# Optimization experiments

Measured on AMD Instinct MI355X. Metric: run time of the kernel, lower is better.

## Reference

```python
import jax, jax.numpy as jnp
import numpy as np

GRID_H, GRID_W = 128, 128
MODES1, MODES2 = 24, 24
DEPTH = 4
WIDTH = 64
IN_CH = 3
OUT_CH = 1
B, N = 8, 16384
EPS = 1e-5


def _gelu(x):
    return jax.nn.gelu(x, approximate=False)  # torch default (erf) GELU


def setup_inputs() -> dict:
    key = jax.random.key(0)
    ks = jax.random.split(key, 16)
    f32 = jnp.float32

    def lin(k, i, o, std=None):
        s = std if std is not None else 1.0 / np.sqrt(i)
        return (jax.random.normal(k, (i, o), f32) * s).astype(f32)

    scale = 1.0 / (WIDTH * WIDTH)
    sw_shape = (DEPTH, WIDTH, WIDTH, MODES1, MODES2)
    return {
        'coords': jax.random.uniform(ks[0], (B, N, 2), f32, -1.0, 1.0),
        'features': jax.random.normal(ks[1], (B, N, IN_CH), f32),
        'dw0': lin(ks[2], 2, 32), 'db0': jnp.zeros((32,), f32),
        'dw1': lin(ks[3], 32, 32), 'db1': jnp.zeros((32,), f32),
        'dw2': lin(ks[4], 32, 2, std=0.01), 'db2': jnp.zeros((2,), f32),
        'lift_w': lin(ks[5], IN_CH + 2, WIDTH), 'lift_b': jnp.zeros((WIDTH,), f32),
        'sw1r': scale * jax.random.uniform(ks[6], sw_shape, f32),
        'sw1i': scale * jax.random.uniform(ks[7], sw_shape, f32),
        'sw2r': scale * jax.random.uniform(ks[8], sw_shape, f32),
        'sw2i': scale * jax.random.uniform(ks[9], sw_shape, f32),
        'pw_w': (jax.random.normal(ks[10], (DEPTH, WIDTH, WIDTH), f32) / np.sqrt(WIDTH)).astype(f32),
        'pw_b': jnp.zeros((DEPTH, WIDTH), f32),
        'p1_w': lin(ks[11], WIDTH, 128), 'p1_b': jnp.zeros((128,), f32),
        'p2_w': lin(ks[12], 128, OUT_CH), 'p2_b': jnp.zeros((OUT_CH,), f32),
    }


def _spectral_conv2d(x, w1, w2):
    # x: (B, C, H, W); w1/w2: (C_in, C_out, MODES1, MODES2) complex
    Bb, C, H, W = x.shape
    x_ft = jnp.fft.rfft2(x)  # (B, C, H, W//2+1)
    lo = jnp.einsum('bixy,ioxy->boxy', x_ft[:, :, :MODES1, :MODES2], w1)
    hi = jnp.einsum('bixy,ioxy->boxy', x_ft[:, :, -MODES1:, :MODES2], w2)
    out_ft = jnp.zeros((Bb, WIDTH, H, W // 2 + 1), jnp.complex64)
    out_ft = out_ft.at[:, :, :MODES1, :MODES2].set(lo)
    out_ft = out_ft.at[:, :, -MODES1:, :MODES2].set(hi)
    return jnp.fft.irfft2(out_ft, s=(H, W))


def _forward(coords, features, dw0, db0, dw1, db1, dw2, db2, lift_w, lift_b,
             sw1r, sw1i, sw2r, sw2i, pw_w, pw_b, p1_w, p1_b, p2_w, p2_b):
    Bb, Nn, _ = coords.shape
    # 1) deformation: latent = x + MLP(x), clamped to [-1, 1]
    h = _gelu(coords @ dw0 + db0)
    h = _gelu(h @ dw1 + db1)
    latent = jnp.clip(coords + (h @ dw2 + db2), -1.0, 1.0)
    # 2) lifting on concat(features, coords)
    feat = jnp.concatenate([features, coords], axis=-1) @ lift_w + lift_b  # (B,N,width)
    # 3) P2G: nearest-neighbor scatter-mean onto latent grid (align_corners=True)
    ph = (latent[..., 0] + 1.0) * 0.5 * (GRID_H - 1)
    pw = (latent[..., 1] + 1.0) * 0.5 * (GRID_W - 1)
    ih = jnp.clip(jnp.round(ph).astype(jnp.int32), 0, GRID_H - 1)
    iw = jnp.clip(jnp.round(pw).astype(jnp.int32), 0, GRID_W - 1)
    boff = jnp.arange(Bb, dtype=jnp.int32)[:, None] * (GRID_H * GRID_W)
    flat = (boff + ih * GRID_W + iw).reshape(-1)
    nseg = Bb * GRID_H * GRID_W
    sums = jax.ops.segment_sum(feat.reshape(-1, WIDTH), flat, num_segments=nseg)
    cnts = jax.ops.segment_sum(jnp.ones((Bb * Nn, 1), feat.dtype), flat, num_segments=nseg)
    grid = (sums / jnp.maximum(cnts, 1.0)).reshape(Bb, GRID_H, GRID_W, WIDTH)
    grid = grid.transpose(0, 3, 1, 2)  # (B, width, H, W)
    # 4) FNO blocks: gelu(instnorm(spectral(x) + pointwise(x)))
    for d in range(DEPTH):
        w1 = sw1r[d] + 1j * sw1i[d]
        w2 = sw2r[d] + 1j * sw2i[d]
        y = _spectral_conv2d(grid, w1, w2)
        y = y + jnp.einsum('bihw,io->bohw', grid, pw_w[d]) + pw_b[d][None, :, None, None]
        mu = y.mean(axis=(2, 3), keepdims=True)
        var = y.var(axis=(2, 3), keepdims=True)
        grid = _gelu((y - mu) * jax.lax.rsqrt(var + EPS))
    # 5) G2P: bilinear sample latent grid at latent coords
    h0 = jnp.floor(ph)
    w0 = jnp.floor(pw)
    th = (ph - h0)[:, None, :]
    tw = (pw - w0)[:, None, :]
    h0i = jnp.clip(h0.astype(jnp.int32), 0, GRID_H - 1)
    h1i = jnp.clip(h0i + 1, 0, GRID_H - 1)
    w0i = jnp.clip(w0.astype(jnp.int32), 0, GRID_W - 1)
    w1i = jnp.clip(w0i + 1, 0, GRID_W - 1)
    gridf = grid.reshape(Bb, WIDTH, GRID_H * GRID_W)

    def gather(hi_, wi_):
        idx = (hi_ * GRID_W + wi_)[:, None, :]  # (B,1,N)
        return jnp.take_along_axis(gridf, idx, axis=2)  # (B,width,N)

    v00 = gather(h0i, w0i)
    v01 = gather(h0i, w1i)
    v10 = gather(h1i, w0i)
    v11 = gather(h1i, w1i)
    sampled = (v00 * (1 - th) * (1 - tw) + v01 * (1 - th) * tw
               + v10 * th * (1 - tw) + v11 * th * tw)
    sampled = sampled.transpose(0, 2, 1)  # (B,N,width)
    # 6) projection (dropout is identity at eval)
    out = _gelu(sampled @ p1_w + p1_b) @ p2_w + p2_b
    return out  # (B, N, out_channels)


def reference(coords, features, dw0, db0, dw1, db1, dw2, db2, lift_w, lift_b,
              sw1r, sw1i, sw2r, sw2i, pw_w, pw_b, p1_w, p1_b, p2_w, p2_b):
    return _forward(coords, features, dw0, db0, dw1, db1, dw2, db2, lift_w, lift_b,
                    sw1r, sw1i, sw2r, sw2i, pw_w, pw_b, p1_w, p1_b, p2_w, p2_b)
```

## Files before the change

kernel.cpp:

```cpp
#include <hip/hip_runtime.h>
#include <math.h>

#define GH 128
#define GW 128
#define HWC 16384
#define NMODE 1152
#define PI_F 3.14159265358979323846f

typedef _Float16 f16;
typedef __attribute__((ext_vector_type(8))) _Float16 f16x8;
typedef __attribute__((ext_vector_type(4))) float f32x4;

__device__ __forceinline__ float gelu_f(float x) {
  return 0.5f * x * (1.0f + erff(x * 0.70710678118654752f));
}

__global__ __launch_bounds__(256) void k_twiddle(f16* __restrict__ Fw, f16* __restrict__ Fh,
                                                 f16* __restrict__ Bh, f16* __restrict__ Bw,
                                                 const float* __restrict__ p1w, f16* __restrict__ p1t)
{
  int idx = blockIdx.x * 256 + threadIdx.x;
  if (idx < 6144) {
    int n = idx >> 7, w = idx & 127;
    int ky = n >> 1;
    int ang = (ky * w) & 127;
    float s, c; sincosf((float)ang * (PI_F / 64.f), &s, &c);
    Fw[idx] = (f16)((n & 1) ? -s : c);
  } else if (idx < 18432) {
    int t = idx - 6144;
    int n = t >> 7, h = t & 127;
    int kx = n < 48 ? n : n - 48;
    int f = kx < 24 ? kx : kx + 80;
    int ang = (f * h) & 127;
    float s, c; sincosf((float)ang * (PI_F / 64.f), &s, &c);
    float v = (n < 48) ? c : s;
    Fh[t] = (f16)v;
    Bh[h * 96 + n] = (f16)v;
  } else if (idx < 26624) {
    int t = idx - 18432;
    int w = t >> 6, k = t & 63;
    float v = 0.f;
    if (k < 48 && k != 1) {
      int ky = k >> 1;
      float g = (ky == 0) ? 1.f : 2.f;
      int ang = (ky * w) & 127;
      float s, c; sincosf((float)ang * (PI_F / 64.f), &s, &c);
      v = (k & 1) ? -g * s : g * c;
    }
    Bw[t] = (f16)v;
  } else if (idx < 34816) {
    int t = idx - 26624;
    int j = t >> 6, i = t & 63;
    p1t[t] = (f16)p1w[i * 128 + j];
  }
}

__global__ __launch_bounds__(256) void k_points(
    const float* __restrict__ coords,
    const float* __restrict__ dw0, const float* __restrict__ db0,
    const float* __restrict__ dw1, const float* __restrict__ db1,
    const float* __restrict__ dw2, const float* __restrict__ db2,
    int* __restrict__ cnt_i,
    int* __restrict__ ptrank, int* __restrict__ pd_cell,
    int* __restrict__ pd_idx, float* __restrict__ pd_th, float* __restrict__ pd_tw)
{
  int pid = blockIdx.x * 256 + threadIdx.x;
  float2 c = ((const float2*)coords)[pid];

  float h1[32];
#pragma unroll
  for (int j = 0; j < 32; ++j)
    h1[j] = gelu_f(fmaf(c.x, dw0[j], fmaf(c.y, dw0[32 + j], db0[j])));

  float a[32];
#pragma unroll
  for (int j = 0; j < 32; ++j) a[j] = db1[j];
#pragma unroll 4
  for (int k = 0; k < 32; ++k) {
    float hk = h1[k];
    const float* wr = dw1 + k * 32;
#pragma unroll
    for (int j = 0; j < 32; ++j) a[j] = fmaf(hk, wr[j], a[j]);
  }

  float d0 = db2[0], d1 = db2[1];
#pragma unroll 4
  for (int k = 0; k < 32; ++k) {
    float hk = gelu_f(a[k]);
    d0 = fmaf(hk, dw2[2 * k], d0);
    d1 = fmaf(hk, dw2[2 * k + 1], d1);
  }

  float l0 = fminf(fmaxf(c.x + d0, -1.f), 1.f);
  float l1 = fminf(fmaxf(c.y + d1, -1.f), 1.f);
  float ph = (l0 + 1.f) * 0.5f * 127.f;
  float pw = (l1 + 1.f) * 0.5f * 127.f;
  int ih = min(max((int)rintf(ph), 0), 127);
  int iw = min(max((int)rintf(pw), 0), 127);
  int b = pid >> 14;
  int cell = b * HWC + ih * GW + iw;

  int r = atomicAdd(&cnt_i[cell], 1);
  ptrank[pid] = r;
  pd_cell[pid] = cell;

  float fh = floorf(ph), fw = floorf(pw);
  int h0i = min(max((int)fh, 0), 127), w0i = min(max((int)fw, 0), 127);
  pd_idx[pid] = h0i | (w0i << 8);
  pd_th[pid] = ph - fh;
  pd_tw[pid] = pw - fw;
}

__global__ __launch_bounds__(256) void k_scanA(const int* __restrict__ cnt,
                                               int* __restrict__ starts, int* __restrict__ btot)
{
  __shared__ int sh[256];
  int blk = blockIdx.x, t = threadIdx.x;
  int base = blk * 512;
  int v0 = cnt[base + 2 * t], v1 = cnt[base + 2 * t + 1];
  int pair = v0 + v1;
  sh[t] = pair; __syncthreads();
  int acc = pair;
  for (int off = 1; off < 256; off <<= 1) {
    int add = (t >= off) ? sh[t - off] : 0;
    __syncthreads();
    acc += add; sh[t] = acc;
    __syncthreads();
  }
  int excl = acc - pair;
  starts[base + 2 * t] = excl;
  starts[base + 2 * t + 1] = excl + v0;
  if (t == 255) btot[blk] = acc;
}

__global__ __launch_bounds__(256) void k_scanB(const int* __restrict__ btot, int* __restrict__ boff)
{
  __shared__ int sh[256];
  int t = threadIdx.x;
  int v = btot[t];
  sh[t] = v; __syncthreads();
  int acc = v;
  for (int off = 1; off < 256; off <<= 1) {
    int add = (t >= off) ? sh[t - off] : 0;
    __syncthreads();
    acc += add; sh[t] = acc;
    __syncthreads();
  }
  boff[t] = acc - v;
}

__global__ __launch_bounds__(256) void k_perm(const int* __restrict__ pd_cell, const int* __restrict__ ptrank,
                                              const int* __restrict__ starts, const int* __restrict__ boff,
                                              const int* __restrict__ pd_idx, const float* __restrict__ pd_th,
                                              const float* __restrict__ pd_tw,
                                              const float* __restrict__ coords, const float* __restrict__ feats,
                                              int4* __restrict__ pds,
                                              float4* __restrict__ scA, float* __restrict__ scB)
{
  int pid = blockIdx.x * 256 + threadIdx.x;
  int cell = pd_cell[pid];
  int dst = starts[cell] + boff[cell >> 9] + ptrank[pid];
  int4 rec;
  rec.x = pid;
  rec.y = pd_idx[pid];
  rec.z = __float_as_int(pd_th[pid]);
  rec.w = __float_as_int(pd_tw[pid]);
  pds[dst] = rec;
  float2 c = ((const float2*)coords)[pid];
  scA[dst] = make_float4(feats[pid * 3], feats[pid * 3 + 1], feats[pid * 3 + 2], c.x);
  scB[dst] = c.y;
}

__global__ __launch_bounds__(256) void k_gridlift(const float4* __restrict__ scA, const float* __restrict__ scB,
                                                  const int* __restrict__ starts, const int* __restrict__ boff,
                                                  const int* __restrict__ cnt_i,
                                                  const float* __restrict__ lw,
                                                  const float* __restrict__ lb,
                                                  f16* __restrict__ Gh)
{
  __shared__ float sp[2][128][5];
  __shared__ float s_lw[5][64];
  __shared__ float s_lb[64];
  __shared__ float s_cnt[128];
  int b = blockIdx.y, cbase = blockIdx.x * 128, tid = threadIdx.x;
  int cl = tid & 127, par = tid >> 7;
  int gcell = b * HWC + cbase + cl;
  int start = starts[gcell] + boff[gcell >> 9];
  int cnt = cnt_i[gcell];
  float a0 = 0.f, a1 = 0.f, a2 = 0.f, a3 = 0.f, a4 = 0.f;
  for (int p = start + par; p < start + cnt; p += 2) {
    float4 A = scA[p];
    a0 += A.x; a1 += A.y; a2 += A.z; a3 += A.w; a4 += scB[p];
  }
  sp[par][cl][0] = a0; sp[par][cl][1] = a1; sp[par][cl][2] = a2;
  sp[par][cl][3] = a3; sp[par][cl][4] = a4;
  if (par == 0) s_cnt[cl] = (float)cnt;
  for (int l = tid; l < 320; l += 256) ((float*)s_lw)[l] = lw[l];
  if (tid < 64) s_lb[tid] = lb[tid];
  __syncthreads();
  float v0 = sp[0][cl][0] + sp[1][cl][0];
  float v1 = sp[0][cl][1] + sp[1][cl][1];
  float v2 = sp[0][cl][2] + sp[1][cl][2];
  float v3 = sp[0][cl][3] + sp[1][cl][3];
  float v4 = sp[0][cl][4] + sp[1][cl][4];
  float cntf = s_cnt[cl];
  float inv = 1.f / fmaxf(cntf, 1.f);
  int oh = tid >> 7;
#pragma unroll
  for (int j = 0; j < 32; ++j) {
    int o = oh * 32 + j;
    float val = cntf * s_lb[o];
    val = fmaf(v0, s_lw[0][o], val);
    val = fmaf(v1, s_lw[1][o], val);
    val = fmaf(v2, s_lw[2][o], val);
    val = fmaf(v3, s_lw[3][o], val);
    val = fmaf(v4, s_lw[4][o], val);
    Gh[(size_t)(b * 64 + o) * HWC + cbase + cl] = (f16)(val * inv);
  }
}

__global__ __launch_bounds__(256) void k_fwdpw(const f16* __restrict__ Gh,
                                               const f16* __restrict__ Fw_t, const f16* __restrict__ Fh_t,
                                               float2* __restrict__ Xf2,
                                               const float* __restrict__ pww, const float* __restrict__ pwb,
                                               f16* __restrict__ yh)
{
  __shared__ char smem[52224];
  int tid = threadIdx.x;
  int wave = tid >> 6, lane = tid & 63, lr = lane & 15, lg = lane >> 4;

  if (blockIdx.x < 512) {
    f16 (*s_fw)[136]  = (f16(*)[136])smem;
    f16 (*s_img)[136] = (f16(*)[136])(smem + 13056);
    f16 (*s_xw)[136]  = (f16(*)[136])(smem + 13056);
    f16 (*s_fh)[136]  = (f16(*)[136])(smem + 13056 + 48 * 136 * 2);
    int bc = blockIdx.x;
    for (int l = tid; l < 2048; l += 256) {
      int r = l >> 4, c = l & 15;
      *(f16x8*)&s_img[r][c * 8] = *(const f16x8*)(Gh + (size_t)bc * HWC + r * 128 + c * 8);
    }
    for (int l = tid; l < 768; l += 256) {
      int r = l >> 4, c = l & 15;
      *(f16x8*)&s_fw[r][c * 8] = *(const f16x8*)(Fw_t + r * 128 + c * 8);
    }
    __syncthreads();

    f32x4 acc1[2][3] = {};
#pragma unroll
    for (int ks = 0; ks < 4; ++ks) {
      f16x8 a[2], b[3];
#pragma unroll
      for (int mm = 0; mm < 2; ++mm) a[mm] = *(const f16x8*)&s_img[(wave * 2 + mm) * 16 + lr][ks * 32 + lg * 8];
#pragma unroll
      for (int nt = 0; nt < 3; ++nt) b[nt] = *(const f16x8*)&s_fw[nt * 16 + lr][ks * 32 + lg * 8];
#pragma unroll
      for (int mm = 0; mm < 2; ++mm)
#pragma unroll
        for (int nt = 0; nt < 3; ++nt)
          acc1[mm][nt] = __builtin_amdgcn_mfma_f32_16x16x32_f16(a[mm], b[nt], acc1[mm][nt], 0, 0, 0);
    }
    __syncthreads();
#pragma unroll
    for (int mm = 0; mm < 2; ++mm)
#pragma unroll
      for (int nt = 0; nt < 3; ++nt) {
        int n = nt * 16 + lr;
        int h0 = (wave * 2 + mm) * 16 + lg * 4;
#pragma unroll
        for (int r = 0; r < 4; ++r) s_xw[n][h0 + r] = (f16)acc1[mm][nt][r];
      }
    for (int l = tid; l < 1536; l += 256) {
      int r = l >> 4, c = l & 15;
      *(f16x8*)&s_fh[r][c * 8] = *(const f16x8*)(Fh_t + r * 128 + c * 8);
    }
    __syncthreads();

    for (int u = wave; u < 9; u += 4) {
      int mt = u / 3, ntC = u - mt * 3;
      f32x4 accC = {}, accS = {};
#pragma unroll
      for (int ks = 0; ks < 4; ++ks) {
        f16x8 a  = *(const f16x8*)&s_xw[mt * 16 + lr][ks * 32 + lg * 8];
        f16x8 bC = *(const f16x8*)&s_fh[ntC * 16 + lr][ks * 32 + lg * 8];
        f16x8 bS = *(const f16x8*)&s_fh[(ntC + 3) * 16 + lr][ks * 32 + lg * 8];
        accC = __builtin_amdgcn_mfma_f32_16x16x32_f16(a, bC, accC, 0, 0, 0);
        accS = __builtin_amdgcn_mfma_f32_16x16x32_f16(a, bS, accS, 0, 0, 0);
      }
      int kx = ntC * 16 + lr;
      int ky0 = (mt * 16 + lg * 4) >> 1;
      Xf2[bc * NMODE + kx * 24 + ky0]     = make_float2(accC[0] + accS[1], accC[1] - accS[0]);
      Xf2[bc * NMODE + kx * 24 + ky0 + 1] = make_float2(accC[2] + accS[3], accC[3] - accS[2]);
    }
  } else {
    f16 (*gt)[72] = (f16(*)[72])smem;
    f16 (*wt)[72] = (f16(*)[72])(smem + 36864);
    float* s_b    = (float*)(smem + 46080);
    int blk = blockIdx.x - 512;
    int b = blk >> 6, p0 = (blk & 63) * 256;
    for (int l = tid; l < 4096; l += 256) {
      int i = l >> 6, o = l & 63;
      wt[o][i ^ (((o >> 3) & 7) << 3)] = (f16)pww[l];
    }
    if (tid < 64) s_b[tid] = pwb[tid];
    for (int l = tid; l < 2048; l += 256) {
      int i = l >> 5, pc = (l & 31) * 8;
      f16x8 v = *(const f16x8*)(Gh + (size_t)(b * 64 + i) * HWC + p0 + pc);
      int sw = (l & 7) << 3;
#pragma unroll
      for (int j = 0; j < 8; ++j) gt[pc + j][i ^ sw] = v[j];
    }
    __syncthreads();
    int pw_ = wave * 64;
    f32x4 acc[4][4] = {};
#pragma unroll
    for (int kk = 0; kk < 2; ++kk) {
      f16x8 a[4], bb[4];
#pragma unroll
      for (int mi = 0; mi < 4; ++mi) {
        int o = 16 * mi + lr;
        a[mi] = *(const f16x8*)&wt[o][(kk * 32 + lg * 8) ^ (((o >> 3) & 7) << 3)];
      }
#pragma unroll
      for (int ni = 0; ni < 4; ++ni) {
        int p = pw_ + 16 * ni + lr;
        bb[ni] = *(const f16x8*)&gt[p][(kk * 32 + lg * 8) ^ (((p >> 3) & 7) << 3)];
      }
#pragma unroll
      for (int mi = 0; mi < 4; ++mi)
#pragma unroll
        for (int ni = 0; ni < 4; ++ni)
          acc[mi][ni] = __builtin_amdgcn_mfma_f32_16x16x32_f16(a[mi], bb[ni], acc[mi][ni], 0, 0, 0);
    }
    __syncthreads();
    f16 (*s_o)[264] = (f16(*)[264])smem;
#pragma unroll
    for (int mi = 0; mi < 4; ++mi)
#pragma unroll
      for (int ni = 0; ni < 4; ++ni) {
#pragma unroll
        for (int r = 0; r < 4; ++r) {
          int o = 16 * mi + lg * 4 + r;
          s_o[o][pw_ + 16 * ni + lr] = (f16)(acc[mi][ni][r] + s_b[o]);
        }
      }
    __syncthreads();
    for (int l = tid; l < 2048; l += 256) {
      int o = l >> 5, pc = (l & 31) * 8;
      *(f16x8*)(yh + (size_t)(b * 64 + o) * HWC + p0 + pc) = *(const f16x8*)&s_o[o][pc];
    }
  }
}

__global__ __launch_bounds__(128) void k_mix(const float2* __restrict__ Xf2,
    const float* __restrict__ w1r, const float* __restrict__ w1i,
    const float* __restrict__ w2r, const float* __restrict__ w2i,
    float2* __restrict__ Yf2)
{
  int m = blockIdx.x * 64 + (threadIdx.x & 63);
  int o = blockIdx.y * 2 + (threadIdx.x >> 6);
  int half = blockIdx.z;
  int gm = half * 576 + m;
  const float* wr_ = half ? w2r : w1r;
  const float* wi_ = half ? w2i : w1i;
  float aR[8] = {}, aI[8] = {};
#pragma unroll 2
  for (int i = 0; i < 64; ++i) {
    int widx = (i * 64 + o) * 576 + m;
    float wr = wr_[widx], wi = wi_[widx];
#pragma unroll
    for (int b = 0; b < 8; ++b) {
      float2 x = Xf2[(b * 64 + i) * NMODE + gm];
      aR[b] = fmaf(x.x, wr, aR[b]); aR[b] = fmaf(-x.y, wi, aR[b]);
      aI[b] = fmaf(x.x, wi, aI[b]); aI[b] = fmaf(x.y, wr, aI[b]);
    }
  }
#pragma unroll
  for (int b = 0; b < 8; ++b)
    Yf2[(b * 64 + o) * NMODE + gm] = make_float2(aR[b], aI[b]);
}

__global__ __launch_bounds__(256) void k_inv(const float2* __restrict__ Yf2,
                                             const f16* __restrict__ Bh_t, const f16* __restrict__ Bw_t,
                                             const f16* __restrict__ yh, f16* __restrict__ Gh)
{
  __shared__ f16 s_u[21120];
  __shared__ float rs[256], rq[256];
  __shared__ float s_mu, s_rstd;
  f16 (*s_a)[120]  = (f16(*)[120])s_u;
  f16 (*s_bh)[120] = (f16(*)[120])(s_u + 48 * 120);
  f16 (*s_t)[72]   = (f16(*)[72])s_u;
  f16 (*s_bw)[72]  = (f16(*)[72])(s_u + 128 * 72);
  f16 (*s_y)[136]  = (f16(*)[136])s_u;
  int bc = blockIdx.x, tid = threadIdx.x;

  for (int l = tid; l < 1152; l += 256) {
    int kx = l / 24, ky = l - kx * 24;
    float2 y = Yf2[bc * NMODE + l];
    s_a[2 * ky][kx]          = (f16)y.x;
    s_a[2 * ky][48 + kx]     = (f16)(-y.y);
    s_a[2 * ky + 1][kx]      = (f16)y.y;
    s_a[2 * ky + 1][48 + kx] = (f16)y.x;
  }
  for (int l = tid; l < 1536; l += 256) {
    int r = l / 12, c = l - r * 12;
    *(f16x8*)&s_bh[r][c * 8] = *(const f16x8*)(Bh_t + r * 96 + c * 8);
  }
  __syncthreads();
  int wave = tid >> 6, lane = tid & 63, lr = lane & 15, lg = lane >> 4;

  f32x4 acc_a[6];
#pragma unroll
  for (int i = 0; i < 6; ++i) acc_a[i] = (f32x4){0.f, 0.f, 0.f, 0.f};
#pragma unroll
  for (int i = 0; i < 6; ++i) {
    int t = wave + 4 * i;
    int mt = t >> 3, nt = t & 7;
#pragma unroll
    for (int ks = 0; ks < 3; ++ks) {
      f16x8 a = *(const f16x8*)&s_a[mt * 16 + lr][ks * 32 + lg * 8];
      f16x8 b = *(const f16x8*)&s_bh[nt * 16 + lr][ks * 32 + lg * 8];
      acc_a[i] = __builtin_amdgcn_mfma_f32_16x16x32_f16(a, b, acc_a[i], 0, 0, 0);
    }
  }
  __syncthreads();
#pragma unroll
  for (int i = 0; i < 6; ++i) {
    int t = wave + 4 * i;
    int mt = t >> 3, nt = t & 7;
    int h = nt * 16 + lr;
    int m0 = mt * 16 + lg * 4;
#pragma unroll
    for (int r = 0; r < 4; ++r) s_t[h][m0 + r] = (f16)acc_a[i][r];
  }
  for (int l = tid; l < 2048; l += 256) {
    int h = l >> 4, c = 48 + (l & 15);
    s_t[h][c] = (f16)0.f;
  }
  for (int l = tid; l < 1024; l += 256) {
    int r = l >> 3, c = l & 7;
    *(f16x8*)&s_bw[r][c * 8] = *(const f16x8*)(Bw_t + r * 64 + c * 8);
  }
  __syncthreads();

  f32x4 acc_b[2][8] = {};
#pragma unroll
  for (int ks = 0; ks < 2; ++ks) {
    f16x8 a[2], b[8];
#pragma unroll
    for (int mm = 0; mm < 2; ++mm) a[mm] = *(const f16x8*)&s_t[(wave * 2 + mm) * 16 + lr][ks * 32 + lg * 8];
#pragma unroll
    for (int nt = 0; nt < 8; ++nt) b[nt] = *(const f16x8*)&s_bw[nt * 16 + lr][ks * 32 + lg * 8];
#pragma unroll
    for (int mm = 0; mm < 2; ++mm)
#pragma unroll
      for (int nt = 0; nt < 8; ++nt)
        acc_b[mm][nt] = __builtin_amdgcn_mfma_f32_16x16x32_f16(a[mm], b[nt], acc_b[mm][nt], 0, 0, 0);
  }
  __syncthreads();
  for (int l = tid; l < 2048; l += 256) {
    int r = l >> 4, c = l & 15;
    *(f16x8*)&s_y[r][c * 8] = *(const f16x8*)(yh + (size_t)bc * HWC + r * 128 + c * 8);
  }
  __syncthreads();
  float sum = 0.f, ssq = 0.f;
#pragma unroll
  for (int mm = 0; mm < 2; ++mm)
#pragma unroll
    for (int nt = 0; nt < 8; ++nt)
#pragma unroll
      for (int r = 0; r < 4; ++r) {
        int h = (wave * 2 + mm) * 16 + lg * 4 + r;
        int w = nt * 16 + lr;
        float v = acc_b[mm][nt][r] * (1.f / 16384.f) + (float)s_y[h][w];
        acc_b[mm][nt][r] = v;
        sum += v; ssq = fmaf(v, v, ssq);
      }
  rs[tid] = sum; rq[tid] = ssq;
  __syncthreads();
  for (int sft = 128; sft > 0; sft >>= 1) {
    if (tid < sft) { rs[tid] += rs[tid + sft]; rq[tid] += rq[tid + sft]; }
    __syncthreads();
  }
  if (tid == 0) {
    float mu = rs[0] * (1.f / 16384.f);
    float var = fmaxf(rq[0] * (1.f / 16384.f) - mu * mu, 0.f);
    s_mu = mu;
    s_rstd = rsqrtf(var + 1e-5f);
  }
  __syncthreads();
  float mu = s_mu, rstd = s_rstd;
#pragma unroll
  for (int mm = 0; mm < 2; ++mm)
#pragma unroll
    for (int nt = 0; nt < 8; ++nt)
#pragma unroll
      for (int r = 0; r < 4; ++r) {
        int h = (wave * 2 + mm) * 16 + lg * 4 + r;
        int w = nt * 16 + lr;
        s_y[h][w] = (f16)gelu_f((acc_b[mm][nt][r] - mu) * rstd);
      }
  __syncthreads();
  for (int l = tid; l < 2048; l += 256) {
    int r = l >> 4, c = l & 15;
    *(f16x8*)(Gh + (size_t)bc * HWC + r * 128 + c * 8) = *(const f16x8*)&s_y[r][c * 8];
  }
}

__global__ __launch_bounds__(256) void k_tr(const f16* __restrict__ Gh, f16* __restrict__ Gp)
{
  __shared__ f16 t[64][264];
  int b = blockIdx.x >> 6, cell0 = (blockIdx.x & 63) * 256, tid = threadIdx.x;
  for (int l = tid; l < 2048; l += 256) {
    int c = l >> 5, q = l & 31;
    *(f16x8*)&t[c][q * 8] = *(const f16x8*)(Gh + (size_t)(b * 64 + c) * HWC + cell0 + q * 8);
  }
  __syncthreads();
  int cell = tid;
  f16* dst = Gp + ((size_t)b * HWC + cell0 + cell) * 64;
#pragma unroll
  for (int q = 0; q < 8; ++q) {
    f16x8 v;
#pragma unroll
    for (int j = 0; j < 8; ++j) v[j] = t[q * 8 + j][cell];
    *(f16x8*)(dst + q * 8) = v;
  }
}

__global__ __launch_bounds__(128) void k_mlp(const f16* __restrict__ Gp,
                                             const int4* __restrict__ pds,
                                             const f16* __restrict__ p1t,
                                             const float* __restrict__ p1b,
                                             const float* __restrict__ p2w, const float* __restrict__ p2b,
                                             float* __restrict__ out)
{
  __shared__ f16 s_in[64][72];
  __shared__ f16 s_p1[128][72];
  __shared__ float s_b1[128], s_p2[128];
  __shared__ unsigned s_c0[64], s_c1[64], s_c2[64], s_c3[64];
  __shared__ float4 s_w[64];
  __shared__ int s_pid[64];
  int blk = blockIdx.x, tid = threadIdx.x;
  if (tid < 64) {
    int4 rec = pds[blk * 64 + tid];
    s_pid[tid] = rec.x;
    int b = rec.x >> 14;
    int h0 = rec.y & 255, w0 = (rec.y >> 8) & 255;
    int h1 = min(h0 + 1, 127), w1 = min(w0 + 1, 127);
    float th = __int_as_float(rec.z), tw = __int_as_float(rec.w);
    unsigned gb = ((unsigned)b << 14) * 64u;
    s_c0[tid] = gb + (unsigned)(h0 * 128 + w0) * 64u;
    s_c1[tid] = gb + (unsigned)(h0 * 128 + w1) * 64u;
    s_c2[tid] = gb + (unsigned)(h1 * 128 + w0) * 64u;
    s_c3[tid] = gb + (unsigned)(h1 * 128 + w1) * 64u;
    s_w[tid] = make_float4((1.f - th) * (1.f - tw), (1.f - th) * tw,
                           th * (1.f - tw), th * tw);
  }
  s_b1[tid] = p1b[tid];
  s_p2[tid] = p2w[tid];
  for (int l = tid; l < 1024; l += 128) {
    int j = l >> 3, c8 = (l & 7) * 8;
    *(f16x8*)&s_p1[j][c8] = *(const f16x8*)(p1t + j * 64 + c8);
  }
  __syncthreads();
  for (int l = tid; l < 512; l += 128) {
    int row = l >> 3, c8 = (l & 7) * 8;
    float4 wv = s_w[row];
    f16x8 a  = *(const f16x8*)(Gp + s_c0[row] + c8);
    f16x8 b2 = *(const f16x8*)(Gp + s_c1[row] + c8);
    f16x8 c  = *(const f16x8*)(Gp + s_c2[row] + c8);
    f16x8 d  = *(const f16x8*)(Gp + s_c3[row] + c8);
    f16x8 o;
#pragma unroll
    for (int j = 0; j < 8; ++j)
      o[j] = (f16)(wv.x * (float)a[j] + wv.y * (float)b2[j] + wv.z * (float)c[j] + wv.w * (float)d[j]);
    *(f16x8*)&s_in[row][c8] = o;
  }
  __syncthreads();
  int wave = tid >> 6, lane = tid & 63, lr = lane & 15, lg = lane >> 4;
  f32x4 acc[2][8] = {};
#pragma unroll
  for (int ks = 0; ks < 2; ++ks) {
    f16x8 a[2], b[8];
#pragma unroll
    for (int mm = 0; mm < 2; ++mm) a[mm] = *(const f16x8*)&s_in[(wave * 2 + mm) * 16 + lr][ks * 32 + lg * 8];
#pragma unroll
    for (int nt = 0; nt < 8; ++nt) b[nt] = *(const f16x8*)&s_p1[nt * 16 + lr][ks * 32 + lg * 8];
#pragma unroll
    for (int mm = 0; mm < 2; ++mm)
#pragma unroll
      for (int nt = 0; nt < 8; ++nt)
        acc[mm][nt] = __builtin_amdgcn_mfma_f32_16x16x32_f16(a[mm], b[nt], acc[mm][nt], 0, 0, 0);
  }
  float p2b0 = p2b[0];
  float part[2][4] = {};
#pragma unroll
  for (int mm = 0; mm < 2; ++mm)
#pragma unroll
    for (int nt = 0; nt < 8; ++nt) {
#pragma unroll
      for (int r = 0; r < 4; ++r) {
        int j = nt * 16 + lr;
        part[mm][r] += gelu_f(acc[mm][nt][r] + s_b1[j]) * s_p2[j];
      }
    }
#pragma unroll
  for (int mm = 0; mm < 2; ++mm)
#pragma unroll
    for (int r = 0; r < 4; ++r) {
      float v = part[mm][r];
      v += __shfl_xor(v, 1, 16);
      v += __shfl_xor(v, 2, 16);
      v += __shfl_xor(v, 4, 16);
      v += __shfl_xor(v, 8, 16);
      if (lr == 0) {
        int pt = (wave * 2 + mm) * 16 + lg * 4 + r;
        out[s_pid[pt]] = v + p2b0;
      }
    }
}

extern "C" void kernel_launch(void* const* d_in, const int* in_sizes, int n_in,
                              void* d_out, int out_size, void* d_ws, size_t ws_size,
                              hipStream_t stream) {
  const float* coords = (const float*)d_in[0];
  const float* feats  = (const float*)d_in[1];
  const float* dw0 = (const float*)d_in[2];
  const float* db0 = (const float*)d_in[3];
  const float* dw1 = (const float*)d_in[4];
  const float* db1 = (const float*)d_in[5];
  const float* dw2 = (const float*)d_in[6];
  const float* db2 = (const float*)d_in[7];
  const float* liftw = (const float*)d_in[8];
  const float* liftb = (const float*)d_in[9];
  const float* sw1r = (const float*)d_in[10];
  const float* sw1i = (const float*)d_in[11];
  const float* sw2r = (const float*)d_in[12];
  const float* sw2i = (const float*)d_in[13];
  const float* pww = (const float*)d_in[14];
  const float* pwb = (const float*)d_in[15];
  const float* p1w = (const float*)d_in[16];
  const float* p1b = (const float*)d_in[17];
  const float* p2w = (const float*)d_in[18];
  const float* p2b = (const float*)d_in[19];
  float* out = (float*)d_out;
  char* base = (char*)d_ws;

  int*    cnt_i  = (int*)(base + 0);
  int*    ptrank = (int*)(base + 524288);
  int*    pd_cell= (int*)(base + 1048576);
  int*    starts = (int*)(base + 1572864);
  int*    btot   = (int*)(base + 2097152);
  int*    boff   = (int*)(base + 2098176);
  int*    pd_idx = (int*)(base + 2099200);
  float*  pd_th  = (float*)(base + 2623488);
  float*  pd_tw  = (float*)(base + 3147776);
  f16*    Gh     = (f16*)(base + 8388608);
  f16*    yh     = (f16*)(base + 25165824);
  float2* Xf2    = (float2*)(base + 41943040);
  float2* Yf2    = (float2*)(base + 46661632);
  int4*   pds    = (int4*)(base + 51380224);
  f16*    Gp     = (f16*)(base + 53477376);
  float4* scA    = (float4*)(base + 70254592);
  float*  scB    = (float*)(base + 72351744);
  f16*    Fw_t   = (f16*)(base + 87031808);
  f16*    Fh_t   = (f16*)(base + 87044096);
  f16*    Bh_t   = (f16*)(base + 87068672);
  f16*    Bw_t   = (f16*)(base + 87093248);
  f16*    p1t    = (f16*)(base + 87109632);

  hipMemsetAsync(cnt_i, 0, 524288, stream);

  k_twiddle<<<136, 256, 0, stream>>>(Fw_t, Fh_t, Bh_t, Bw_t, p1w, p1t);
  k_points<<<512, 256, 0, stream>>>(coords, dw0, db0, dw1, db1, dw2, db2,
                                    cnt_i, ptrank, pd_cell, pd_idx, pd_th, pd_tw);
  k_scanA<<<256, 256, 0, stream>>>(cnt_i, starts, btot);
  k_scanB<<<1, 256, 0, stream>>>(btot, boff);
  k_perm<<<512, 256, 0, stream>>>(pd_cell, ptrank, starts, boff, pd_idx, pd_th, pd_tw,
                                  coords, feats, pds, scA, scB);
  k_gridlift<<<dim3(128, 8), 256, 0, stream>>>(scA, scB, starts, boff, cnt_i, liftw, liftb, Gh);

  for (int d = 0; d < 4; ++d) {
    const int swoff = d * 2359296;
    k_fwdpw<<<1024, 256, 0, stream>>>(Gh, Fw_t, Fh_t, Xf2, pww + d * 4096, pwb + d * 64, yh);
    k_mix<<<dim3(9, 32, 2), 128, 0, stream>>>(Xf2, sw1r + swoff, sw1i + swoff,
                                              sw2r + swoff, sw2i + swoff, Yf2);
    k_inv<<<512, 256, 0, stream>>>(Yf2, Bh_t, Bw_t, yh, Gh);
  }

  k_tr<<<512, 256, 0, stream>>>(Gh, Gp);
  k_mlp<<<2048, 128, 0, stream>>>(Gp, pds, p1t, p1b, p2w, p2b, out);
}
```

Measured before the change: 383.2 us.

## Split bilinear gather out of MLP kernel into separate gather kernel

Moves the bilinear grid sampling into its own fully parallel kernel that writes sampled f16 features to a workspace buffer, which reuses the yh region. The MLP kernel then loads contiguous rows and processes 128 points per 256-thread block instead of 64 per 128. The goal is more memory-level parallelism for the random gathers and less serialized work inside the MFMA kernel. The cost is an extra launch plus a round trip of the sampled tensor through global memory.

```diff
diff --git a/kernel.cpp b/kernel.cpp
--- a/kernel.cpp
+++ b/kernel.cpp
@@ -526,55 +526,51 @@
   }
 }
 
-__global__ __launch_bounds__(128) void k_mlp(const f16* __restrict__ Gp,
+__global__ __launch_bounds__(256) void k_gather(const f16* __restrict__ Gp,
+                                                const int4* __restrict__ pds,
+                                                f16* __restrict__ smp)
+{
+  int idx = blockIdx.x * 256 + threadIdx.x;
+  int spt = idx >> 3, c8 = (idx & 7) * 8;
+  int4 rec = pds[spt];
+  int b = rec.x >> 14;
+  int h0 = rec.y & 255, w0 = (rec.y >> 8) & 255;
+  int h1 = min(h0 + 1, 127), w1 = min(w0 + 1, 127);
+  float th = __int_as_float(rec.z), tw = __int_as_float(rec.w);
+  float w00 = (1.f - th) * (1.f - tw), w01 = (1.f - th) * tw;
+  float w10 = th * (1.f - tw), w11 = th * tw;
+  const f16* base = Gp + (((size_t)b << 14) << 6);
+  f16x8 a  = *(const f16x8*)(base + (h0 * 128 + w0) * 64 + c8);
+  f16x8 b2 = *(const f16x8*)(base + (h0 * 128 + w1) * 64 + c8);
+  f16x8 c  = *(const f16x8*)(base + (h1 * 128 + w0) * 64 + c8);
+  f16x8 d  = *(const f16x8*)(base + (h1 * 128 + w1) * 64 + c8);
+  f16x8 o;
+#pragma unroll
+  for (int j = 0; j < 8; ++j)
+    o[j] = (f16)(w00 * (float)a[j] + w01 * (float)b2[j] + w10 * (float)c[j] + w11 * (float)d[j]);
+  *(f16x8*)(smp + (size_t)spt * 64 + c8) = o;
+}
+
+__global__ __launch_bounds__(256) void k_mlp(const f16* __restrict__ smp,
                                              const int4* __restrict__ pds,
                                              const f16* __restrict__ p1t,
                                              const float* __restrict__ p1b,
                                              const float* __restrict__ p2w, const float* __restrict__ p2b,
                                              float* __restrict__ out)
 {
-  __shared__ f16 s_in[64][72];
+  __shared__ f16 s_in[128][72];
   __shared__ f16 s_p1[128][72];
   __shared__ float s_b1[128], s_p2[128];
-  __shared__ unsigned s_c0[64], s_c1[64], s_c2[64], s_c3[64];
-  __shared__ float4 s_w[64];
-  __shared__ int s_pid[64];
   int blk = blockIdx.x, tid = threadIdx.x;
-  if (tid < 64) {
-    int4 rec = pds[blk * 64 + tid];
-    s_pid[tid] = rec.x;
-    int b = rec.x >> 14;
-    int h0 = rec.y & 255, w0 = (rec.y >> 8) & 255;
-    int h1 = min(h0 + 1, 127), w1 = min(w0 + 1, 127);
-    float th = __int_as_float(rec.z), tw = __int_as_float(rec.w);
-    unsigned gb = ((unsigned)b << 14) * 64u;
-    s_c0[tid] = gb + (unsigned)(h0 * 128 + w0) * 64u;
-    s_c1[tid] = gb + (unsigned)(h0 * 128 + w1) * 64u;
-    s_c2[tid] = gb + (unsigned)(h1 * 128 + w0) * 64u;
-    s_c3[tid] = gb + (unsigned)(h1 * 128 + w1) * 64u;
-    s_w[tid] = make_float4((1.f - th) * (1.f - tw), (1.f - th) * tw,
-                           th * (1.f - tw), th * tw);
-  }
-  s_b1[tid] = p1b[tid];
-  s_p2[tid] = p2w[tid];
-  for (int l = tid; l < 1024; l += 128) {
+  for (int l = tid; l < 1024; l += 256) {
+    int row = l >> 3, c8 = (l & 7) * 8;
+    *(f16x8*)&s_in[row][c8] = *(const f16x8*)(smp + ((size_t)blk * 128 + row) * 64 + c8);
+  }
+  for (int l = tid; l < 1024; l += 256) {
     int j = l >> 3, c8 = (l & 7) * 8;
     *(f16x8*)&s_p1[j][c8] = *(const f16x8*)(p1t + j * 64 + c8);
   }
-  __syncthreads();
-  for (int l = tid; l < 512; l += 128) {
-    int row = l >> 3, c8 = (l & 7) * 8;
-    float4 wv = s_w[row];
-    f16x8 a  = *(const f16x8*)(Gp + s_c0[row] + c8);
-    f16x8 b2 = *(const f16x8*)(Gp + s_c1[row] + c8);
-    f16x8 c  = *(const f16x8*)(Gp + s_c2[row] + c8);
-    f16x8 d  = *(const f16x8*)(Gp + s_c3[row] + c8);
-    f16x8 o;
-#pragma unroll
-    for (int j = 0; j < 8; ++j)
-      o[j] = (f16)(wv.x * (float)a[j] + wv.y * (float)b2[j] + wv.z * (float)c[j] + wv.w * (float)d[j]);
-    *(f16x8*)&s_in[row][c8] = o;
-  }
+  if (tid < 128) { s_b1[tid] = p1b[tid]; s_p2[tid] = p2w[tid]; }
   __syncthreads();
   int wave = tid >> 6, lane = tid & 63, lr = lane & 15, lg = lane >> 4;
   f32x4 acc[2][8] = {};
@@ -614,7 +610,8 @@
       v += __shfl_xor(v, 8, 16);
       if (lr == 0) {
         int pt = (wave * 2 + mm) * 16 + lg * 4 + r;
-        out[s_pid[pt]] = v + p2b0;
+        int opid = pds[blk * 128 + pt].x;
+        out[opid] = v + p2b0;
       }
     }
 }
@@ -656,6 +653,7 @@
   float*  pd_tw  = (float*)(base + 3147776);
   f16*    Gh     = (f16*)(base + 8388608);
   f16*    yh     = (f16*)(base + 25165824);
+  f16*    smp    = (f16*)(base + 25165824);
   float2* Xf2    = (float2*)(base + 41943040);
   float2* Yf2    = (float2*)(base + 46661632);
   int4*   pds    = (int4*)(base + 51380224);
@@ -688,5 +686,6 @@
   }
 
   k_tr<<<512, 256, 0, stream>>>(Gh, Gp);
-  k_mlp<<<2048, 128, 0, stream>>>(Gp, pds, p1t, p1b, p2w, p2b, out);
-}
+  k_gather<<<4096, 256, 0, stream>>>(Gp, pds, smp);
+  k_mlp<<<1024, 256, 0, stream>>>(smp, pds, p1t, p1b, p2w, p2b, out);
+}
```

Result: no change. 389.3 us (+1.6%).
